# Kernel optimization log

Hardware: AMD Instinct MI355X
Metric: run time of the kernel (lower is better)

## Reference

```python
import jax, jax.numpy as jnp
import numpy as np

EPS = 1e-5      # batch-norm epsilon
ALPHA = 0.2     # leaky_relu negative slope


def bn_lrelu(h, gamma, beta):
    # training-mode batch norm over the batch axis, then leaky relu
    mean = jnp.mean(h, axis=0)
    var = jnp.var(h, axis=0)
    h = (h - mean) * jax.lax.rsqrt(var + EPS) * gamma + beta
    return jnp.where(h >= 0, h, ALPHA * h)


def setup_inputs() -> dict:
    key = jax.random.key(0)
    ks = jax.random.split(key, 16)
    O, T, Din, H, Dout = 50000, 200000, 128, 512, 128
    s = 0.02
    inp = {
        "obj_vecs": jax.random.normal(ks[0], (O, Din), jnp.float32),
        "pred_vecs": jax.random.normal(ks[1], (T, Din), jnp.float32),
        "edges": jax.random.randint(ks[2], (T, 2), 0, O, jnp.int64),
        # net1: [3*Din -> H -> 2H+Dout], each Linear followed by BN + leaky_relu
        "W1a": jax.random.normal(ks[3], (3 * Din, H), jnp.float32) * s,
        "b1a": jnp.zeros((H,), jnp.float32),
        "g1a": jnp.ones((H,), jnp.float32),
        "be1a": jnp.zeros((H,), jnp.float32),
        "W1b": jax.random.normal(ks[4], (H, 2 * H + Dout), jnp.float32) * s,
        "b1b": jnp.zeros((2 * H + Dout,), jnp.float32),
        "g1b": jnp.ones((2 * H + Dout,), jnp.float32),
        "be1b": jnp.zeros((2 * H + Dout,), jnp.float32),
        # net2: [H -> H -> Dout]
        "W2a": jax.random.normal(ks[5], (H, H), jnp.float32) * s,
        "b2a": jnp.zeros((H,), jnp.float32),
        "g2a": jnp.ones((H,), jnp.float32),
        "be2a": jnp.zeros((H,), jnp.float32),
        "W2b": jax.random.normal(ks[6], (H, Dout), jnp.float32) * s,
        "b2b": jnp.zeros((Dout,), jnp.float32),
        "g2b": jnp.ones((Dout,), jnp.float32),
        "be2b": jnp.zeros((Dout,), jnp.float32),
    }
    return inp


def reference(obj_vecs, pred_vecs, edges,
              W1a, b1a, g1a, be1a, W1b, b1b, g1b, be1b,
              W2a, b2a, g2a, be2a, W2b, b2b, g2b, be2b):
    O = obj_vecs.shape[0]
    H = W1a.shape[1]
    Dout = W2b.shape[1]
    s_idx = edges[:, 0]
    o_idx = edges[:, 1]

    # gather subject/object vecs and concat with predicate vecs: [T, 3*Din]
    cur_t = jnp.concatenate([obj_vecs[s_idx], pred_vecs, obj_vecs[o_idx]], axis=1)

    # net1 MLP
    h = bn_lrelu(cur_t @ W1a + b1a, g1a, be1a)           # [T, H]
    new_t = bn_lrelu(h @ W1b + b1b, g1b, be1b)            # [T, 2H+Dout]

    new_s = new_t[:, :H]
    new_p = new_t[:, H:H + Dout]
    new_o = new_t[:, H + Dout:]

    # scatter-add pooling back to objects, then average
    pooled = jnp.zeros((O, H), jnp.float32).at[s_idx].add(new_s).at[o_idx].add(new_o)
    counts = jnp.zeros((O,), jnp.float32).at[s_idx].add(1.0).at[o_idx].add(1.0)
    counts = jnp.clip(counts, 1.0, float(O))
    pooled = pooled / counts[:, None]

    # net2 MLP
    h2 = bn_lrelu(pooled @ W2a + b2a, g2a, be2a)          # [O, H]
    new_obj = bn_lrelu(h2 @ W2b + b2b, g2b, be2b)         # [O, Dout]
    return new_obj, new_p
```

## Files before the change

kernel.cpp:

```cpp
#include <hip/hip_runtime.h>

typedef __bf16 bf16;
typedef __bf16 bf16x8 __attribute__((ext_vector_type(8)));
typedef float  f32x4  __attribute__((ext_vector_type(4)));

#define BM 128
#define BN 128
#define BKT 64
#define LDK (BKT + 8)

template<int AMODE, int EPI>
__global__ __launch_bounds__(256) void gemm_k(
    const bf16* __restrict__ Abf, const float* __restrict__ Af32,
    const float* __restrict__ obj, const float* __restrict__ pred,
    const int* __restrict__ edges, const float* __restrict__ invcnt,
    const float* __restrict__ scale, const float* __restrict__ shift,
    const float* __restrict__ oscale, const float* __restrict__ oshift,
    const bf16* __restrict__ WT,
    bf16* __restrict__ outB, float* __restrict__ outF,
    float* __restrict__ pooled, float* __restrict__ gsum, float* __restrict__ gsq,
    int M, int N, int K)
{
  __shared__ __align__(16) bf16 As[BM][LDK];
  __shared__ __align__(16) bf16 Bs[BN][LDK];
  __shared__ float sc_sh[(AMODE == 1) ? 512 : 1];
  __shared__ float sh_sh[(AMODE == 1) ? 512 : 1];
  __shared__ float osc[(EPI == 2) ? BN : 1];
  __shared__ float osh[(EPI == 2) ? BN : 1];
  __shared__ int eS[(AMODE == 0 || EPI == 2) ? BM : 1];
  __shared__ int eO[(AMODE == 0 || EPI == 2) ? BM : 1];

  const int tid = threadIdx.x;
  const int m0 = blockIdx.x * BM;
  const int n0 = blockIdx.y * BN;
  const int lane = tid & 63;
  const int w = tid >> 6;
  const int wm = (w >> 1) * 64;
  const int wn = (w & 1) * 64;
  const int l15 = lane & 15;
  const int quad = lane >> 4;

  if (AMODE == 1) {
    for (int c = tid; c < K; c += 256) { sc_sh[c] = scale[c]; sh_sh[c] = shift[c]; }
  }
  if (EPI == 2) {
    if (tid < BN) { osc[tid] = oscale[n0 + tid]; osh[tid] = oshift[n0 + tid]; }
  }
  if (AMODE == 0 || EPI == 2) {
    if (tid < BM) {
      int r = m0 + tid; if (r >= M) r = M - 1;
      eS[tid] = edges[2 * r];
      eO[tid] = edges[2 * r + 1];
    }
  }
  __syncthreads();

  f32x4 acc[4][4];
  #pragma unroll
  for (int i = 0; i < 4; ++i)
    #pragma unroll
    for (int j = 0; j < 4; ++j)
      acc[i][j] = (f32x4){0.f, 0.f, 0.f, 0.f};

  for (int k0 = 0; k0 < K; k0 += BKT) {
    {
      int idx = tid;
      #pragma unroll
      for (int it = 0; it < 4; ++it, idx += 256) {
        int r = idx >> 3, c8 = (idx & 7) << 3;
        bf16x8 v = *reinterpret_cast<const bf16x8*>(WT + (size_t)(n0 + r) * K + k0 + c8);
        *reinterpret_cast<bf16x8*>(&Bs[r][c8]) = v;
      }
    }
    if (AMODE == 1 || AMODE == 3) {
      int idx = tid;
      #pragma unroll
      for (int it = 0; it < 4; ++it, idx += 256) {
        int r = idx >> 3, c8 = (idx & 7) << 3;
        int row = m0 + r; if (row >= M) row = M - 1;
        bf16x8 v = *reinterpret_cast<const bf16x8*>(Abf + (size_t)row * K + k0 + c8);
        if (AMODE == 1) {
          bf16x8 o;
          #pragma unroll
          for (int e = 0; e < 8; ++e) {
            int c = k0 + c8 + e;
            float f = sc_sh[c] * (float)v[e] + sh_sh[c];
            f = f >= 0.f ? f : 0.2f * f;
            o[e] = (bf16)f;
          }
          *reinterpret_cast<bf16x8*>(&As[r][c8]) = o;
        } else {
          *reinterpret_cast<bf16x8*>(&As[r][c8]) = v;
        }
      }
    } else {
      int idx = tid;
      #pragma unroll
      for (int it = 0; it < 8; ++it, idx += 256) {
        int r = idx >> 4, c4 = (idx & 15) << 2;
        int row = m0 + r; if (row >= M) row = M - 1;
        const float* src;
        float mul = 1.f;
        if (AMODE == 0) {
          int k = k0 + c4;
          if (k < 128)      src = obj  + (size_t)eS[r] * 128 + k;
          else if (k < 256) src = pred + (size_t)row * 128 + (k - 128);
          else              src = obj  + (size_t)eO[r] * 128 + (k - 256);
        } else {
          src = Af32 + (size_t)row * K + k0 + c4;
          mul = invcnt[row];
        }
        float4 v = *reinterpret_cast<const float4*>(src);
        As[r][c4 + 0] = (bf16)(v.x * mul);
        As[r][c4 + 1] = (bf16)(v.y * mul);
        As[r][c4 + 2] = (bf16)(v.z * mul);
        As[r][c4 + 3] = (bf16)(v.w * mul);
      }
    }
    __syncthreads();
    #pragma unroll
    for (int kk = 0; kk < BKT; kk += 32) {
      bf16x8 af[4], bfv[4];
      #pragma unroll
      for (int i = 0; i < 4; ++i)
        af[i] = *reinterpret_cast<const bf16x8*>(&As[wm + i * 16 + l15][kk + quad * 8]);
      #pragma unroll
      for (int j = 0; j < 4; ++j)
        bfv[j] = *reinterpret_cast<const bf16x8*>(&Bs[wn + j * 16 + l15][kk + quad * 8]);
      #pragma unroll
      for (int i = 0; i < 4; ++i)
        #pragma unroll
        for (int j = 0; j < 4; ++j)
          acc[i][j] = __builtin_amdgcn_mfma_f32_16x16x32_bf16(af[i], bfv[j], acc[i][j], 0, 0, 0);
    }
    __syncthreads();
  }

  if (EPI == 2) {
    #pragma unroll
    for (int i = 0; i < 4; ++i) {
      #pragma unroll
      for (int r = 0; r < 4; ++r) {
        int lrow = wm + i * 16 + quad * 4 + r;
        int row = m0 + lrow;
        if (row >= M) continue;
        #pragma unroll
        for (int j = 0; j < 4; ++j) {
          int cl = wn + j * 16 + l15;
          int n1 = n0 + cl;
          float v = osc[cl] * acc[i][j][r] + osh[cl];
          v = v >= 0.f ? v : 0.2f * v;
          if (n1 < 512)      atomicAdd(&pooled[(size_t)eS[lrow] * 512 + n1], v);
          else if (n1 < 640) outF[(size_t)row * 128 + (n1 - 512)] = v;
          else               atomicAdd(&pooled[(size_t)eO[lrow] * 512 + (n1 - 640)], v);
        }
      }
    }
  } else {
    #pragma unroll
    for (int j = 0; j < 4; ++j) {
      float s = 0.f, q = 0.f;
      #pragma unroll
      for (int i = 0; i < 4; ++i) {
        #pragma unroll
        for (int r = 0; r < 4; ++r) {
          int row = m0 + wm + i * 16 + quad * 4 + r;
          if (row >= M) continue;
          float v = acc[i][j][r];
          s += v; q += v * v;
          int col = n0 + wn + j * 16 + l15;
          if (EPI == 0) outB[(size_t)row * N + col] = (bf16)v;
          if (EPI == 3) outF[(size_t)row * N + col] = v;
        }
      }
      s += __shfl_xor(s, 16); q += __shfl_xor(q, 16);
      s += __shfl_xor(s, 32); q += __shfl_xor(q, 32);
      if (quad == 0) {
        int col = n0 + wn + j * 16 + l15;
        atomicAdd(&gsum[col], s);
        atomicAdd(&gsq[col], q);
      }
    }
  }
}

__global__ __launch_bounds__(256) void tconv_k(const float* __restrict__ W,
                                               bf16* __restrict__ WT, int K, int N) {
  int idx = blockIdx.x * 256 + threadIdx.x;
  if (idx < K * N) {
    int n = idx / K, k = idx - n * K;
    WT[(size_t)n * K + k] = (bf16)W[(size_t)k * N + n];
  }
}

__global__ __launch_bounds__(256) void bnfin_k(const float* __restrict__ sum,
    const float* __restrict__ sq, const float* __restrict__ g,
    const float* __restrict__ be, float* __restrict__ scale,
    float* __restrict__ shift, int C, float invR) {
  int c = blockIdx.x * 256 + threadIdx.x;
  if (c < C) {
    float m = sum[c] * invR;
    float v = sq[c] * invR - m * m;
    float a = g[c] * rsqrtf(v + 1e-5f);
    scale[c] = a;
    shift[c] = be[c] - m * a;
  }
}

__global__ __launch_bounds__(256) void cntint_k(const int* __restrict__ edges,
                                                int* __restrict__ cnt, int T) {
  int t = blockIdx.x * 256 + threadIdx.x;
  if (t < T) {
    atomicAdd(&cnt[edges[2 * t]], 1);
    atomicAdd(&cnt[edges[2 * t + 1]], 1);
  }
}

__global__ __launch_bounds__(256) void invcnt_k(const int* __restrict__ cnt,
                                                float* __restrict__ invc, int O) {
  int i = blockIdx.x * 256 + threadIdx.x;
  if (i < O) {
    float c = fminf(fmaxf((float)cnt[i], 1.f), (float)O);
    invc[i] = 1.f / c;
  }
}

__global__ __launch_bounds__(1024) void scan_k(const int* __restrict__ cnt,
    int* __restrict__ rowptr, int* __restrict__ head, int O, int total) {
  __shared__ int sh[1024];
  const int t = threadIdx.x;
  const int C = (O + 1023) / 1024;
  const int i0 = t * C;
  int s = 0;
  for (int i = 0; i < C; ++i) { int idx = i0 + i; if (idx < O) s += cnt[idx]; }
  sh[t] = s;
  __syncthreads();
  for (int d = 1; d < 1024; d <<= 1) {
    int v = (t >= d) ? sh[t - d] : 0;
    __syncthreads();
    sh[t] += v;
    __syncthreads();
  }
  int run = (t == 0) ? 0 : sh[t - 1];
  for (int i = 0; i < C; ++i) {
    int idx = i0 + i;
    if (idx < O) { rowptr[idx] = run; head[idx] = run; run += cnt[idx]; }
  }
  if (t == 0) rowptr[O] = total;
}

__global__ __launch_bounds__(256) void fill_k(const int* __restrict__ edges,
    int* __restrict__ head, int* __restrict__ list, int T) {
  int t = blockIdx.x * 256 + threadIdx.x;
  if (t < T) {
    int s = edges[2 * t];
    int p = atomicAdd(&head[s], 1);
    list[p] = t << 1;
    int o = edges[2 * t + 1];
    p = atomicAdd(&head[o], 1);
    list[p] = (t << 1) | 1;
  }
}

__global__ __launch_bounds__(256) void act_k(bf16* __restrict__ hA,
    const float* __restrict__ scale, const float* __restrict__ shift, size_t n8) {
  size_t i = (size_t)blockIdx.x * 256 + threadIdx.x;
  if (i < n8) {
    size_t idx8 = i * 8;
    int c = (int)(idx8 & 511);
    bf16x8 v = *reinterpret_cast<const bf16x8*>(hA + idx8);
    bf16x8 o;
    #pragma unroll
    for (int j = 0; j < 8; ++j) {
      float f = scale[c + j] * (float)v[j] + shift[c + j];
      f = f >= 0.f ? f : 0.2f * f;
      o[j] = (bf16)f;
    }
    *reinterpret_cast<bf16x8*>(hA + idx8) = o;
  }
}

__global__ __launch_bounds__(256) void newp_k(const bf16* __restrict__ tB,
    const float* __restrict__ scale, const float* __restrict__ shift,
    float* __restrict__ outP, int T) {
  int i = blockIdx.x * 256 + threadIdx.x;
  if (i < T * 128) {
    int t = i >> 7, c = i & 127;
    float v = scale[512 + c] * (float)tB[(size_t)t * 1152 + 512 + c] + shift[512 + c];
    outP[i] = v >= 0.f ? v : 0.2f * v;
  }
}

__global__ __launch_bounds__(256) void gather_k(const bf16* __restrict__ tB,
    const int* __restrict__ rowptr, const int* __restrict__ list,
    const float* __restrict__ scale, const float* __restrict__ shift,
    const float* __restrict__ invc, bf16* __restrict__ pooled, int O) {
  int o = blockIdx.x * 4 + (threadIdx.x >> 6);
  if (o >= O) return;
  int lane = threadIdx.x & 63;
  int c0 = lane * 8;
  float scS[8], shS[8], scO[8], shO[8];
  #pragma unroll
  for (int j = 0; j < 8; ++j) {
    scS[j] = scale[c0 + j];       shS[j] = shift[c0 + j];
    scO[j] = scale[640 + c0 + j]; shO[j] = shift[640 + c0 + j];
  }
  float acc[8];
  #pragma unroll
  for (int j = 0; j < 8; ++j) acc[j] = 0.f;
  int e0 = rowptr[o], e1 = rowptr[o + 1];
  for (int e = e0; e < e1; ++e) {
    int id = list[e];
    int t = id >> 1;
    int role = id & 1;
    const bf16* row = tB + (size_t)t * 1152 + (role ? 640 : 0) + c0;
    bf16x8 v = *reinterpret_cast<const bf16x8*>(row);
    if (role) {
      #pragma unroll
      for (int j = 0; j < 8; ++j) {
        float f = scO[j] * (float)v[j] + shO[j];
        acc[j] += (f >= 0.f ? f : 0.2f * f);
      }
    } else {
      #pragma unroll
      for (int j = 0; j < 8; ++j) {
        float f = scS[j] * (float)v[j] + shS[j];
        acc[j] += (f >= 0.f ? f : 0.2f * f);
      }
    }
  }
  float ic = invc[o];
  bf16x8 out;
  #pragma unroll
  for (int j = 0; j < 8; ++j) out[j] = (bf16)(acc[j] * ic);
  *reinterpret_cast<bf16x8*>(pooled + (size_t)o * 512 + c0) = out;
}

__global__ __launch_bounds__(256) void final_k(float* __restrict__ buf,
    const float* __restrict__ scale, const float* __restrict__ shift, int n) {
  int i = blockIdx.x * 256 + threadIdx.x;
  if (i < n) {
    int c = i & 127;
    float v = scale[c] * buf[i] + shift[c];
    buf[i] = v >= 0.f ? v : 0.2f * v;
  }
}

extern "C" void kernel_launch(void* const* d_in, const int* in_sizes, int n_in,
                              void* d_out, int out_size, void* d_ws, size_t ws_size,
                              hipStream_t stream) {
  const float* obj   = (const float*)d_in[0];
  const float* pred  = (const float*)d_in[1];
  const int*   edges = (const int*)d_in[2];
  const float* W1a = (const float*)d_in[3];
  const float* g1a = (const float*)d_in[5];
  const float* be1a= (const float*)d_in[6];
  const float* W1b = (const float*)d_in[7];
  const float* g1b = (const float*)d_in[9];
  const float* be1b= (const float*)d_in[10];
  const float* W2a = (const float*)d_in[11];
  const float* g2a = (const float*)d_in[13];
  const float* be2a= (const float*)d_in[14];
  const float* W2b = (const float*)d_in[15];
  const float* g2b = (const float*)d_in[17];
  const float* be2b= (const float*)d_in[18];

  const int O = in_sizes[0] / 128;
  const int T = in_sizes[1] / 128;
  float* out_obj = (float*)d_out;
  float* out_p   = (float*)d_out + (size_t)O * 128;

  char* base = (char*)d_ws;
  size_t off = 0;
  auto alloc = [&](size_t bytes) { size_t p = off; off += (bytes + 255) & ~(size_t)255; return p; };
  size_t oWT1a = alloc((size_t)384 * 512 * 2);
  size_t oWT1b = alloc((size_t)512 * 1152 * 2);
  size_t oWT2a = alloc((size_t)512 * 512 * 2);
  size_t oWT2b = alloc((size_t)512 * 128 * 2);
  size_t oSums = alloc(4608 * 4);
  size_t oScl  = alloc(4608 * 4);
  size_t oCntI = alloc((size_t)O * 4);
  size_t oInvc = alloc((size_t)O * 4);
  size_t oRp   = alloc((size_t)(O + 1) * 4);
  size_t oHead = alloc((size_t)O * 4);
  size_t oList = alloc((size_t)2 * T * 4);
  size_t oHA   = alloc((size_t)T * 512 * 2);
  size_t oBig  = off;
  size_t need_staged = oBig + (((size_t)T * 1152 * 2 + 255) & ~(size_t)255)
                            + (size_t)O * 512 * 2;
  size_t need_fb     = oBig + (size_t)O * 512 * 4;
  const bool staged = (ws_size >= need_staged);

  bf16* WT1a = (bf16*)(base + oWT1a);
  bf16* WT1b = (bf16*)(base + oWT1b);
  bf16* WT2a = (bf16*)(base + oWT2a);
  bf16* WT2b = (bf16*)(base + oWT2b);
  float* sums = (float*)(base + oSums);
  float* sumA = sums,        * sqA = sums + 512;
  float* sumB = sums + 1024, * sqB = sums + 2176;
  float* sumC = sums + 3328, * sqC = sums + 3840;
  float* sumD = sums + 4352, * sqD = sums + 4480;
  float* scl = (float*)(base + oScl);
  float* scaleA = scl,        * shiftA = scl + 512;
  float* scaleB = scl + 1024, * shiftB = scl + 2176;
  float* scaleC = scl + 3328, * shiftC = scl + 3840;
  float* scaleD = scl + 4352, * shiftD = scl + 4480;
  int*   cntI = (int*)(base + oCntI);
  float* invc = (float*)(base + oInvc);
  int*   rowptr = (int*)(base + oRp);
  int*   head = (int*)(base + oHead);
  int*   list = (int*)(base + oList);
  bf16*  hA = (bf16*)(base + oHA);
  bf16*  h2 = (bf16*)(base + oHA);
  bf16*  tB = (bf16*)(base + oBig);
  bf16*  pooledB = (bf16*)(base + oBig + (((size_t)T * 1152 * 2 + 255) & ~(size_t)255));
  float* pooledF = (float*)(base + oBig);
  float* objpre = out_obj;

  hipMemsetAsync(sums, 0, 4608 * 4, stream);
  hipMemsetAsync(cntI, 0, (size_t)O * 4, stream);

  tconv_k<<<(384 * 512 + 255) / 256, 256, 0, stream>>>(W1a, WT1a, 384, 512);
  tconv_k<<<(512 * 1152 + 255) / 256, 256, 0, stream>>>(W1b, WT1b, 512, 1152);
  tconv_k<<<(512 * 512 + 255) / 256, 256, 0, stream>>>(W2a, WT2a, 512, 512);
  tconv_k<<<(512 * 128 + 255) / 256, 256, 0, stream>>>(W2b, WT2b, 512, 128);
  cntint_k<<<(T + 255) / 256, 256, 0, stream>>>(edges, cntI, T);
  invcnt_k<<<(O + 255) / 256, 256, 0, stream>>>(cntI, invc, O);
  if (staged) {
    scan_k<<<1, 1024, 0, stream>>>(cntI, rowptr, head, O, 2 * T);
    fill_k<<<(T + 255) / 256, 256, 0, stream>>>(edges, head, list, T);
  }

  {
    dim3 g((T + BM - 1) / BM, 512 / BN);
    gemm_k<0, 0><<<g, 256, 0, stream>>>(nullptr, nullptr, obj, pred, edges, nullptr,
        nullptr, nullptr, nullptr, nullptr, WT1a, hA, nullptr, nullptr, sumA, sqA,
        T, 512, 384);
  }
  bnfin_k<<<2, 256, 0, stream>>>(sumA, sqA, g1a, be1a, scaleA, shiftA, 512, 1.f / T);

  act_k<<<(int)(((size_t)T * 512 / 8 + 255) / 256), 256, 0, stream>>>(hA, scaleA, shiftA,
      (size_t)T * 512 / 8);

  if (staged) {
    {
      dim3 g((T + BM - 1) / BM, 1152 / BN);
      gemm_k<3, 0><<<g, 256, 0, stream>>>(hA, nullptr, nullptr, nullptr, nullptr, nullptr,
          nullptr, nullptr, nullptr, nullptr, WT1b, tB, nullptr, nullptr, sumB, sqB,
          T, 1152, 512);
    }
    bnfin_k<<<5, 256, 0, stream>>>(sumB, sqB, g1b, be1b, scaleB, shiftB, 1152, 1.f / T);

    newp_k<<<(T * 128 + 255) / 256, 256, 0, stream>>>(tB, scaleB, shiftB, out_p, T);
    gather_k<<<(O + 3) / 4, 256, 0, stream>>>(tB, rowptr, list, scaleB, shiftB, invc,
        pooledB, O);

    {
      dim3 g((O + BM - 1) / BM, 512 / BN);
      gemm_k<3, 0><<<g, 256, 0, stream>>>(pooledB, nullptr, nullptr, nullptr, nullptr,
          nullptr, nullptr, nullptr, nullptr, nullptr, WT2a, h2, nullptr, nullptr,
          sumC, sqC, O, 512, 512);
    }
  } else {
    hipMemsetAsync(pooledF, 0, (size_t)O * 512 * 4, stream);
    {
      dim3 g((T + BM - 1) / BM, 1152 / BN);
      gemm_k<3, 1><<<g, 256, 0, stream>>>(hA, nullptr, nullptr, nullptr, nullptr, nullptr,
          nullptr, nullptr, nullptr, nullptr, WT1b, nullptr, nullptr, nullptr, sumB, sqB,
          T, 1152, 512);
    }
    bnfin_k<<<5, 256, 0, stream>>>(sumB, sqB, g1b, be1b, scaleB, shiftB, 1152, 1.f / T);
    {
      dim3 g((T + BM - 1) / BM, 1152 / BN);
      gemm_k<3, 2><<<g, 256, 0, stream>>>(hA, nullptr, nullptr, nullptr, edges, nullptr,
          nullptr, nullptr, scaleB, shiftB, WT1b, nullptr, out_p, pooledF, nullptr,
          nullptr, T, 1152, 512);
    }
    {
      dim3 g((O + BM - 1) / BM, 512 / BN);
      gemm_k<2, 0><<<g, 256, 0, stream>>>(nullptr, pooledF, nullptr, nullptr, nullptr,
          invc, nullptr, nullptr, nullptr, nullptr, WT2a, h2, nullptr, nullptr,
          sumC, sqC, O, 512, 512);
    }
  }
  bnfin_k<<<2, 256, 0, stream>>>(sumC, sqC, g2a, be2a, scaleC, shiftC, 512, 1.f / O);

  {
    dim3 g((O + BM - 1) / BM, 128 / BN);
    gemm_k<1, 3><<<g, 256, 0, stream>>>(h2, nullptr, nullptr, nullptr, nullptr, nullptr,
        scaleC, shiftC, nullptr, nullptr, WT2b, nullptr, objpre, nullptr, sumD, sqD,
        O, 128, 512);
  }
  bnfin_k<<<1, 256, 0, stream>>>(sumD, sqD, g2b, be2b, scaleD, shiftD, 128, 1.f / O);

  final_k<<<((size_t)O * 128 + 255) / 256, 256, 0, stream>>>(objpre, scaleD, shiftD,
      (int)((size_t)O * 128));
}
```

Measured before the change: 2.159 ms.

## Compute second-layer BN statistics via Gram matrix and swap GEMM grid axes

In the non-staged path, the per-column BN statistics of h@W1b are no longer found by a full GEMM pass. Instead they come from the column sums and the 512x512 Gram matrix of the activated hA, contracted with W1b. This removes one of the two large T x 1152 GEMM passes, at the cost of atomics on the Gram matrix and an E[x^2]-m^2 variance formula. Separately, every GEMM grid now puts the N tiles on blockIdx.x, so blocks sharing the same A rows are scheduled close together for better L2 reuse.

Result: no change. 2.189 ms (+1.4%).

```diff
diff --git a/kernel.cpp b/kernel.cpp
--- a/kernel.cpp
+++ b/kernel.cpp
@@ -8,6 +8,7 @@
 #define BN 128
 #define BKT 64
 #define LDK (BKT + 8)
+#define LDT 72
 
 template<int AMODE, int EPI>
 __global__ __launch_bounds__(256) void gemm_k(
@@ -31,8 +32,8 @@
   __shared__ int eO[(AMODE == 0 || EPI == 2) ? BM : 1];
 
   const int tid = threadIdx.x;
-  const int m0 = blockIdx.x * BM;
-  const int n0 = blockIdx.y * BN;
+  const int m0 = blockIdx.y * BM;
+  const int n0 = blockIdx.x * BN;
   const int lane = tid & 63;
   const int w = tid >> 6;
   const int wm = (w >> 1) * 64;
@@ -184,6 +185,185 @@
   }
 }
 
+__global__ __launch_bounds__(256) void gram_k(const bf16* __restrict__ A2,
+                                              float* __restrict__ G, int T) {
+  __shared__ __align__(16) bf16 Ks[2][128][LDT];
+  const int tid = threadIdx.x;
+  const int tile = blockIdx.x & 15;
+  const int s    = blockIdx.x >> 4;
+  const int NS   = gridDim.x >> 4;
+  const int k1b = tile >> 2, k2b = tile & 3;
+  const int lane = tid & 63;
+  const int w = tid >> 6;
+  const int wm = (w >> 1) * 64;
+  const int wn = (w & 1) * 64;
+  const int l15 = lane & 15;
+  const int quad = lane >> 4;
+
+  const int NG = (T + 63) >> 6;
+  const int GPB = (NG + NS - 1) / NS;
+  const int g0 = s * GPB;
+  const int gend = min(NG, g0 + GPB);
+
+  f32x4 acc[4][4];
+  #pragma unroll
+  for (int i = 0; i < 4; ++i)
+    #pragma unroll
+    for (int j = 0; j < 4; ++j)
+      acc[i][j] = (f32x4){0.f, 0.f, 0.f, 0.f};
+
+  const int bsel = (k1b == k2b) ? 0 : 1;
+
+  for (int g = g0; g < gend; ++g) {
+    const int t0 = g << 6;
+    #pragma unroll
+    for (int it = 0; it < 4; ++it) {
+      int lin = it * 256 + tid;
+      int t = lin >> 4, c8 = lin & 15;
+      int row = t0 + t;
+      bf16x8 v;
+      #pragma unroll
+      for (int e = 0; e < 8; ++e) v[e] = (bf16)0.f;
+      if (row < T)
+        v = *reinterpret_cast<const bf16x8*>(A2 + (size_t)row * 512 + k1b * 128 + c8 * 8);
+      int ts = t ^ ((c8 & 7) << 3);
+      #pragma unroll
+      for (int e = 0; e < 8; ++e) Ks[0][c8 * 8 + e][ts] = v[e];
+    }
+    if (bsel) {
+      #pragma unroll
+      for (int it = 0; it < 4; ++it) {
+        int lin = it * 256 + tid;
+        int t = lin >> 4, c8 = lin & 15;
+        int row = t0 + t;
+        bf16x8 v;
+        #pragma unroll
+        for (int e = 0; e < 8; ++e) v[e] = (bf16)0.f;
+        if (row < T)
+          v = *reinterpret_cast<const bf16x8*>(A2 + (size_t)row * 512 + k2b * 128 + c8 * 8);
+        int ts = t ^ ((c8 & 7) << 3);
+        #pragma unroll
+        for (int e = 0; e < 8; ++e) Ks[1][c8 * 8 + e][ts] = v[e];
+      }
+    }
+    __syncthreads();
+    #pragma unroll
+    for (int kk = 0; kk < 64; kk += 32) {
+      bf16x8 af[4], bfv[4];
+      #pragma unroll
+      for (int i = 0; i < 4; ++i) {
+        int r = wm + i * 16 + l15;
+        int toff = (kk + quad * 8) ^ (((r >> 3) & 7) << 3);
+        af[i] = *reinterpret_cast<const bf16x8*>(&Ks[0][r][toff]);
+      }
+      #pragma unroll
+      for (int j = 0; j < 4; ++j) {
+        int r = wn + j * 16 + l15;
+        int toff = (kk + quad * 8) ^ (((r >> 3) & 7) << 3);
+        bfv[j] = *reinterpret_cast<const bf16x8*>(&Ks[bsel][r][toff]);
+      }
+      #pragma unroll
+      for (int i = 0; i < 4; ++i)
+        #pragma unroll
+        for (int j = 0; j < 4; ++j)
+          acc[i][j] = __builtin_amdgcn_mfma_f32_16x16x32_bf16(af[i], bfv[j], acc[i][j], 0, 0, 0);
+    }
+    __syncthreads();
+  }
+
+  #pragma unroll
+  for (int i = 0; i < 4; ++i) {
+    #pragma unroll
+    for (int r = 0; r < 4; ++r) {
+      int grow = k1b * 128 + wm + i * 16 + quad * 4 + r;
+      #pragma unroll
+      for (int j = 0; j < 4; ++j) {
+        int gcol = k2b * 128 + wn + j * 16 + l15;
+        atomicAdd(&G[(size_t)grow * 512 + gcol], acc[i][j][r]);
+      }
+    }
+  }
+}
+
+__global__ __launch_bounds__(256) void act_colsum_k(bf16* __restrict__ hA,
+    const float* __restrict__ scale, const float* __restrict__ shift,
+    float* __restrict__ csum, int T) {
+  __shared__ float sh[4 * 512];
+  const int tid = threadIdx.x;
+  const int c0 = (tid & 63) * 8;
+  const int rofs = tid >> 6;
+  float sc[8], sf[8];
+  #pragma unroll
+  for (int j = 0; j < 8; ++j) { sc[j] = scale[c0 + j]; sf[j] = shift[c0 + j]; }
+  float acc[8];
+  #pragma unroll
+  for (int j = 0; j < 8; ++j) acc[j] = 0.f;
+  for (int r = blockIdx.x * 4 + rofs; r < T; r += gridDim.x * 4) {
+    bf16x8 v = *reinterpret_cast<const bf16x8*>(hA + (size_t)r * 512 + c0);
+    bf16x8 o;
+    #pragma unroll
+    for (int j = 0; j < 8; ++j) {
+      float f = sc[j] * (float)v[j] + sf[j];
+      f = f >= 0.f ? f : 0.2f * f;
+      o[j] = (bf16)f;
+      acc[j] += (float)o[j];
+    }
+    *reinterpret_cast<bf16x8*>(hA + (size_t)r * 512 + c0) = o;
+  }
+  #pragma unroll
+  for (int j = 0; j < 8; ++j) sh[rofs * 512 + c0 + j] = acc[j];
+  __syncthreads();
+  for (int c = tid; c < 512; c += 256) {
+    float s = sh[c] + sh[512 + c] + sh[1024 + c] + sh[1536 + c];
+    atomicAdd(&csum[c], s);
+  }
+}
+
+__global__ __launch_bounds__(256) void colstat_k(const float* __restrict__ G,
+    const float* __restrict__ csum, const float* __restrict__ W1b,
+    float* __restrict__ sumB, float* __restrict__ sqB) {
+  __shared__ float wL[4][512];
+  __shared__ float rq[4][4], rs[4][4];
+  const int tid = threadIdx.x;
+  const int c0 = blockIdx.x * 4;
+  for (int idx = tid; idx < 2048; idx += 256) {
+    int c = idx >> 9, k = idx & 511;
+    wL[c][k] = W1b[(size_t)k * 1152 + c0 + c];
+  }
+  __syncthreads();
+  float pq[4] = {0.f, 0.f, 0.f, 0.f};
+  float ps[4] = {0.f, 0.f, 0.f, 0.f};
+  for (int e = tid; e < 512 * 512; e += 256) {
+    int i = e >> 9, j = e & 511;
+    float g = G[e];
+    #pragma unroll
+    for (int c = 0; c < 4; ++c) pq[c] += g * wL[c][i] * wL[c][j];
+  }
+  for (int k = tid; k < 512; k += 256) {
+    float cs = csum[k];
+    #pragma unroll
+    for (int c = 0; c < 4; ++c) ps[c] += cs * wL[c][k];
+  }
+  #pragma unroll
+  for (int c = 0; c < 4; ++c) {
+    #pragma unroll
+    for (int off = 32; off > 0; off >>= 1) {
+      pq[c] += __shfl_xor(pq[c], off);
+      ps[c] += __shfl_xor(ps[c], off);
+    }
+  }
+  const int w = tid >> 6, lane = tid & 63;
+  if (lane == 0) {
+    #pragma unroll
+    for (int c = 0; c < 4; ++c) { rq[w][c] = pq[c]; rs[w][c] = ps[c]; }
+  }
+  __syncthreads();
+  if (tid < 4) {
+    sqB[c0 + tid]  = rq[0][tid] + rq[1][tid] + rq[2][tid] + rq[3][tid];
+    sumB[c0 + tid] = rs[0][tid] + rs[1][tid] + rs[2][tid] + rs[3][tid];
+  }
+}
+
 __global__ __launch_bounds__(256) void tconv_k(const float* __restrict__ W,
                                                bf16* __restrict__ WT, int K, int N) {
   int idx = blockIdx.x * 256 + threadIdx.x;
@@ -379,6 +559,8 @@
   size_t oWT2b = alloc((size_t)512 * 128 * 2);
   size_t oSums = alloc(4608 * 4);
   size_t oScl  = alloc(4608 * 4);
+  size_t oG    = alloc((size_t)512 * 512 * 4);
+  size_t oCsum = alloc(512 * 4);
   size_t oCntI = alloc((size_t)O * 4);
   size_t oInvc = alloc((size_t)O * 4);
   size_t oRp   = alloc((size_t)(O + 1) * 4);
@@ -388,7 +570,6 @@
   size_t oBig  = off;
   size_t need_staged = oBig + (((size_t)T * 1152 * 2 + 255) & ~(size_t)255)
                             + (size_t)O * 512 * 2;
-  size_t need_fb     = oBig + (size_t)O * 512 * 4;
   const bool staged = (ws_size >= need_staged);
 
   bf16* WT1a = (bf16*)(base + oWT1a);
@@ -405,6 +586,8 @@
   float* scaleB = scl + 1024, * shiftB = scl + 2176;
   float* scaleC = scl + 3328, * shiftC = scl + 3840;
   float* scaleD = scl + 4352, * shiftD = scl + 4480;
+  float* Gm   = (float*)(base + oG);
+  float* csum = (float*)(base + oCsum);
   int*   cntI = (int*)(base + oCntI);
   float* invc = (float*)(base + oInvc);
   int*   rowptr = (int*)(base + oRp);
@@ -419,6 +602,10 @@
 
   hipMemsetAsync(sums, 0, 4608 * 4, stream);
   hipMemsetAsync(cntI, 0, (size_t)O * 4, stream);
+  if (!staged) {
+    hipMemsetAsync(Gm, 0, (size_t)512 * 512 * 4, stream);
+    hipMemsetAsync(csum, 0, 512 * 4, stream);
+  }
 
   tconv_k<<<(384 * 512 + 255) / 256, 256, 0, stream>>>(W1a, WT1a, 384, 512);
   tconv_k<<<(512 * 1152 + 255) / 256, 256, 0, stream>>>(W1b, WT1b, 512, 1152);
@@ -431,20 +618,22 @@
     fill_k<<<(T + 255) / 256, 256, 0, stream>>>(edges, head, list, T);
   }
 
+  const int Tb = (T + BM - 1) / BM;
+  const int Ob = (O + BM - 1) / BM;
+
   {
-    dim3 g((T + BM - 1) / BM, 512 / BN);
+    dim3 g(512 / BN, Tb);
     gemm_k<0, 0><<<g, 256, 0, stream>>>(nullptr, nullptr, obj, pred, edges, nullptr,
         nullptr, nullptr, nullptr, nullptr, WT1a, hA, nullptr, nullptr, sumA, sqA,
         T, 512, 384);
   }
   bnfin_k<<<2, 256, 0, stream>>>(sumA, sqA, g1a, be1a, scaleA, shiftA, 512, 1.f / T);
 
-  act_k<<<(int)(((size_t)T * 512 / 8 + 255) / 256), 256, 0, stream>>>(hA, scaleA, shiftA,
-      (size_t)T * 512 / 8);
-
   if (staged) {
+    act_k<<<(int)(((size_t)T * 512 / 8 + 255) / 256), 256, 0, stream>>>(hA, scaleA,
+        shiftA, (size_t)T * 512 / 8);
     {
-      dim3 g((T + BM - 1) / BM, 1152 / BN);
+      dim3 g(1152 / BN, Tb);
       gemm_k<3, 0><<<g, 256, 0, stream>>>(hA, nullptr, nullptr, nullptr, nullptr, nullptr,
           nullptr, nullptr, nullptr, nullptr, WT1b, tB, nullptr, nullptr, sumB, sqB,
           T, 1152, 512);
@@ -456,28 +645,25 @@
         pooledB, O);
 
     {
-      dim3 g((O + BM - 1) / BM, 512 / BN);
+      dim3 g(512 / BN, Ob);
       gemm_k<3, 0><<<g, 256, 0, stream>>>(pooledB, nullptr, nullptr, nullptr, nullptr,
           nullptr, nullptr, nullptr, nullptr, nullptr, WT2a, h2, nullptr, nullptr,
           sumC, sqC, O, 512, 512);
     }
   } else {
     hipMemsetAsync(pooledF, 0, (size_t)O * 512 * 4, stream);
-    {
-      dim3 g((T + BM - 1) / BM, 1152 / BN);
-      gemm_k<3, 1><<<g, 256, 0, stream>>>(hA, nullptr, nullptr, nullptr, nullptr, nullptr,
-          nullptr, nullptr, nullptr, nullptr, WT1b, nullptr, nullptr, nullptr, sumB, sqB,
-          T, 1152, 512);
-    }
+    act_colsum_k<<<1024, 256, 0, stream>>>(hA, scaleA, shiftA, csum, T);
+    gram_k<<<512, 256, 0, stream>>>(hA, Gm, T);
+    colstat_k<<<288, 256, 0, stream>>>(Gm, csum, W1b, sumB, sqB);
     bnfin_k<<<5, 256, 0, stream>>>(sumB, sqB, g1b, be1b, scaleB, shiftB, 1152, 1.f / T);
     {
-      dim3 g((T + BM - 1) / BM, 1152 / BN);
+      dim3 g(1152 / BN, Tb);
       gemm_k<3, 2><<<g, 256, 0, stream>>>(hA, nullptr, nullptr, nullptr, edges, nullptr,
           nullptr, nullptr, scaleB, shiftB, WT1b, nullptr, out_p, pooledF, nullptr,
           nullptr, T, 1152, 512);
     }
     {
-      dim3 g((O + BM - 1) / BM, 512 / BN);
+      dim3 g(512 / BN, Ob);
       gemm_k<2, 0><<<g, 256, 0, stream>>>(nullptr, pooledF, nullptr, nullptr, nullptr,
           invc, nullptr, nullptr, nullptr, nullptr, WT2a, h2, nullptr, nullptr,
           sumC, sqC, O, 512, 512);
@@ -486,7 +672,7 @@
   bnfin_k<<<2, 256, 0, stream>>>(sumC, sqC, g2a, be2a, scaleC, shiftC, 512, 1.f / O);
 
   {
-    dim3 g((O + BM - 1) / BM, 128 / BN);
+    dim3 g(128 / BN, Ob);
     gemm_k<1, 3><<<g, 256, 0, stream>>>(h2, nullptr, nullptr, nullptr, nullptr, nullptr,
         scaleC, shiftC, nullptr, nullptr, WT2b, nullptr, objpre, nullptr, sumD, sqD,
         O, 128, 512);
```
